# Kernel optimization log

Measured on AMD Instinct MI355X. Metric: run time of the kernel, lower is better.

Reference implementation:

```python
import jax, jax.numpy as jnp
import numpy as np


def setup_inputs() -> dict:
    key = jax.random.key(0)
    k1, k2, k3, k4 = jax.random.split(key, 4)
    B, D, C, N = 8192, 2048, 2048, 8
    x = jax.random.normal(k1, (B, D), dtype=jnp.float32)
    W = jax.random.normal(k2, (N, C, D), dtype=jnp.float32) * (1.0 / np.sqrt(D))
    b = jax.random.normal(k3, (N, C), dtype=jnp.float32) * 0.02
    factor = jnp.full((N,), 1.0 / N, dtype=jnp.float32)
    return {"x": x, "W": W, "b": b, "factor": factor}


def reference(x, W, b, factor):
    # Per-head linear: heads[b, n, c] = x @ W[n].T + b[n]
    heads = jnp.einsum("bd,ncd->bnc", x, W) + b[None, :, :]
    # Weighted sum over heads with canonical_factor (torch: cat(...,-1) @ factor)
    out = jnp.einsum("bnc,n->bc", heads, factor)
    return out
```

## Files before the change

### kernel.cpp

```cpp
#include <hip/hip_runtime.h>


#define MDIM 8192
#define KDIM 2048
#define NDIM 2048
#define NHEADS 8

#define BM 128
#define BN 128
#define BK 64

#define WBLKS 1024
#define XBLKS 1024
#define BBLKS 8

using bf16x8 = __attribute__((ext_vector_type(8))) short;
using f32x4  = __attribute__((ext_vector_type(4))) float;
using f4v    = __attribute__((ext_vector_type(4))) float;

__device__ __forceinline__ unsigned short f2bf(float x) {
    unsigned int u = __float_as_uint(x);
    u += 0x7FFFu + ((u >> 16) & 1u);
    return (unsigned short)(u >> 16);
}

__device__ __forceinline__ void async_load16(const void* g, void* l) {
    __builtin_amdgcn_global_load_lds(
        (const __attribute__((address_space(1))) unsigned int*)g,
        (__attribute__((address_space(3))) unsigned int*)l,
        16, 0, 0);
}

__global__ __launch_bounds__(256) void prep_kernel(
        const float* __restrict__ x,
        const float* __restrict__ W,
        const float* __restrict__ b,
        const float* __restrict__ factor,
        unsigned short* __restrict__ xbf,
        unsigned short* __restrict__ Wbf,
        float* __restrict__ beff) {
    const int blk = blockIdx.x;
    const int tid = threadIdx.x;
    if (blk < WBLKS) {
        const size_t CD   = (size_t)NDIM * KDIM;
        const int    nthr = WBLKS * 256;
        const int    c0   = blk * 256 + tid;
        float f[NHEADS];
#pragma unroll
        for (int n = 0; n < NHEADS; ++n) f[n] = factor[n];
        f4v v[4][NHEADS];
#pragma unroll
        for (int it = 0; it < 4; ++it) {
            size_t idx = ((size_t)(c0 + it * nthr)) * 4;
#pragma unroll
            for (int n = 0; n < NHEADS; ++n)
                v[it][n] = __builtin_nontemporal_load(
                    reinterpret_cast<const f4v*>(W + (size_t)n * CD + idx));
        }
#pragma unroll
        for (int it = 0; it < 4; ++it) {
            size_t idx = ((size_t)(c0 + it * nthr)) * 4;
            float ax = 0.f, ay = 0.f, az = 0.f, aw = 0.f;
#pragma unroll
            for (int n = 0; n < NHEADS; ++n) {
                ax += f[n] * v[it][n].x; ay += f[n] * v[it][n].y;
                az += f[n] * v[it][n].z; aw += f[n] * v[it][n].w;
            }
            ushort4 o;
            o.x = f2bf(ax); o.y = f2bf(ay); o.z = f2bf(az); o.w = f2bf(aw);
            *reinterpret_cast<ushort4*>(Wbf + idx) = o;
        }
    } else if (blk < WBLKS + XBLKS) {
        const int nthr = XBLKS * 256;
        const int c0   = (blk - WBLKS) * 256 + tid;
#pragma unroll
        for (int it = 0; it < 16; it += 4) {
            f4v v[4];
#pragma unroll
            for (int j = 0; j < 4; ++j)
                v[j] = *reinterpret_cast<const f4v*>(
                    x + ((size_t)(c0 + (it + j) * nthr)) * 4);
#pragma unroll
            for (int j = 0; j < 4; ++j) {
                size_t idx = ((size_t)(c0 + (it + j) * nthr)) * 4;
                ushort4 o;
                o.x = f2bf(v[j].x); o.y = f2bf(v[j].y);
                o.z = f2bf(v[j].z); o.w = f2bf(v[j].w);
                *reinterpret_cast<ushort4*>(xbf + idx) = o;
            }
        }
    } else {
        int c = (blk - WBLKS - XBLKS) * 256 + tid;
        float s = 0.f;
#pragma unroll
        for (int n = 0; n < NHEADS; ++n) s += factor[n] * b[(size_t)n * NDIM + c];
        beff[c] = s;
    }
}

__global__ __launch_bounds__(256) void gemm_bt_kernel(
    const unsigned short* __restrict__ A,
    const unsigned short* __restrict__ B,
    const float* __restrict__ bias,
    float* __restrict__ C)
{
    __shared__ unsigned short As[BM * BK];
    __shared__ unsigned short Bs[BN * BK];

    const int tid  = threadIdx.x;
    const int lane = tid & 63;
    const int w    = tid >> 6;
    const int m16  = lane & 15;
    const int quad = lane >> 4;

    const int bid = blockIdx.x;
    const int g   = bid >> 3;
    const int nt  = (bid & 7) * 2 + (g & 1);
    const int mt  = g >> 1;
    const int blockN0 = nt * BN;
    const int blockM0 = mt * BM;

    const int wr = (w >> 1) * 64;
    const int wc = (w & 1) * 64;

    const int srow = lane >> 3;
    const int scol = ((lane & 7) ^ srow) * 8;
    const unsigned short* aP[4];
    const unsigned short* bP[4];
    unsigned short* aL[4];
    unsigned short* bL[4];
#pragma unroll
    for (int i = 0; i < 4; ++i) {
        int r = i * 32 + w * 8;
        aP[i] = A + (size_t)(blockM0 + r + srow) * KDIM + scol;
        bP[i] = B + (size_t)(blockN0 + r + srow) * KDIM + scol;
        aL[i] = As + (size_t)r * BK;
        bL[i] = Bs + (size_t)r * BK;
    }

    f32x4 acc[4][4] = {};

    for (int k0 = 0; k0 < KDIM; k0 += BK) {
#pragma unroll
        for (int i = 0; i < 4; ++i) {
            async_load16(aP[i], aL[i]);
            async_load16(bP[i], bL[i]);
            aP[i] += BK; bP[i] += BK;
        }
        __syncthreads();

#pragma unroll
        for (int kk = 0; kk < BK; kk += 32) {
            bf16x8 af[4], bfr[4];
#pragma unroll
            for (int rt = 0; rt < 4; ++rt) {
                int row = wr + rt * 16 + m16;
                int gA = ((kk >> 3) + quad) ^ (row & 7);
                af[rt] = *reinterpret_cast<const bf16x8*>(&As[(size_t)row * BK + gA * 8]);
            }
#pragma unroll
            for (int ct = 0; ct < 4; ++ct) {
                int row = wc + ct * 16 + m16;
                int gB = ((kk >> 3) + quad) ^ (row & 7);
                bfr[ct] = *reinterpret_cast<const bf16x8*>(&Bs[(size_t)row * BK + gB * 8]);
            }
#pragma unroll
            for (int rt = 0; rt < 4; ++rt)
#pragma unroll
                for (int ct = 0; ct < 4; ++ct)
                    acc[rt][ct] = __builtin_amdgcn_mfma_f32_16x16x32_bf16(
                        af[rt], bfr[ct], acc[rt][ct], 0, 0, 0);
        }
        __syncthreads();
    }

    float bv[4];
#pragma unroll
    for (int ct = 0; ct < 4; ++ct) bv[ct] = bias[blockN0 + wc + ct * 16 + m16];
#pragma unroll
    for (int rt = 0; rt < 4; ++rt) {
        int row0 = blockM0 + wr + rt * 16 + quad * 4;
#pragma unroll
        for (int ct = 0; ct < 4; ++ct) {
            int col = blockN0 + wc + ct * 16 + m16;
#pragma unroll
            for (int r = 0; r < 4; ++r)
                C[(size_t)(row0 + r) * NDIM + col] = acc[rt][ct][r] + bv[ct];
        }
    }
}

extern "C" void kernel_launch(void* const* d_in, const int* in_sizes, int n_in,
                              void* d_out, int out_size, void* d_ws, size_t ws_size,
                              hipStream_t stream) {
    const float* x      = (const float*)d_in[0];
    const float* W      = (const float*)d_in[1];
    const float* b      = (const float*)d_in[2];
    const float* factor = (const float*)d_in[3];
    float* out = (float*)d_out;

    unsigned short* xbf  = (unsigned short*)d_ws;
    unsigned short* Wbf  = (unsigned short*)((char*)d_ws + 33554432);
    float*          beff = (float*)((char*)d_ws + 33554432 + 8388608);

    prep_kernel<<<dim3(WBLKS + XBLKS + BBLKS), dim3(256), 0, stream>>>(
        x, W, b, factor, xbf, Wbf, beff);
    gemm_bt_kernel<<<dim3(1024), dim3(256), 0, stream>>>(xbf, Wbf, beff, out);
}
```

Baseline: 325.9 us.

## Triple-buffer GEMM LDS tiles with 256x128 blocks and 512 threads

Rewrites the bf16 GEMM around a 3-stage LDS ring that prefetches two K-tiles ahead using async global-to-LDS loads. It replaces the two __syncthreads per iteration with one vmcnt wait plus a barrier, so memory latency overlaps the MFMA work. The block tile grows to 256x128 with 8 waves of 8x2 MFMA tiles each, giving more reuse per loaded tile. The nontemporal hint is also dropped from the W loads in the prep kernel. The ring uses about 147KB of LDS, which limits each CU to one block and leaves only 512 blocks in the grid.

```diff
diff --git a/kernel.cpp b/kernel.cpp
--- a/kernel.cpp
+++ b/kernel.cpp
@@ -6,9 +6,12 @@
 #define NDIM 2048
 #define NHEADS 8
 
-#define BM 128
+#define BM 256
 #define BN 128
 #define BK 64
+#define NT (KDIM / BK)
+#define ABUF_ELEMS (BM * BK)
+#define BBUF_ELEMS (BN * BK)
 
 #define WBLKS 1024
 #define XBLKS 1024
@@ -54,8 +57,7 @@
             size_t idx = ((size_t)(c0 + it * nthr)) * 4;
 #pragma unroll
             for (int n = 0; n < NHEADS; ++n)
-                v[it][n] = __builtin_nontemporal_load(
-                    reinterpret_cast<const f4v*>(W + (size_t)n * CD + idx));
+                v[it][n] = *reinterpret_cast<const f4v*>(W + (size_t)n * CD + idx);
         }
 #pragma unroll
         for (int it = 0; it < 4; ++it) {
@@ -98,20 +100,21 @@
     }
 }
 
-__global__ __launch_bounds__(256) void gemm_bt_kernel(
+__global__ __launch_bounds__(512) void gemm_bt_kernel(
     const unsigned short* __restrict__ A,
     const unsigned short* __restrict__ B,
     const float* __restrict__ bias,
     float* __restrict__ C)
 {
-    __shared__ unsigned short As[BM * BK];
-    __shared__ unsigned short Bs[BN * BK];
+    __shared__ unsigned short ring[3][ABUF_ELEMS + BBUF_ELEMS];
 
     const int tid  = threadIdx.x;
     const int lane = tid & 63;
     const int w    = tid >> 6;
     const int m16  = lane & 15;
     const int quad = lane >> 4;
+    const int wm   = w >> 2;
+    const int wn   = w & 3;
 
     const int bid = blockIdx.x;
     const int g   = bid >> 3;
@@ -120,69 +123,89 @@
     const int blockN0 = nt * BN;
     const int blockM0 = mt * BM;
 
-    const int wr = (w >> 1) * 64;
-    const int wc = (w & 1) * 64;
-
     const int srow = lane >> 3;
     const int scol = ((lane & 7) ^ srow) * 8;
     const unsigned short* aP[4];
-    const unsigned short* bP[4];
-    unsigned short* aL[4];
-    unsigned short* bL[4];
-#pragma unroll
-    for (int i = 0; i < 4; ++i) {
-        int r = i * 32 + w * 8;
-        aP[i] = A + (size_t)(blockM0 + r + srow) * KDIM + scol;
-        bP[i] = B + (size_t)(blockN0 + r + srow) * KDIM + scol;
-        aL[i] = As + (size_t)r * BK;
-        bL[i] = Bs + (size_t)r * BK;
-    }
-
-    f32x4 acc[4][4] = {};
-
-    for (int k0 = 0; k0 < KDIM; k0 += BK) {
-#pragma unroll
-        for (int i = 0; i < 4; ++i) {
-            async_load16(aP[i], aL[i]);
-            async_load16(bP[i], bL[i]);
-            aP[i] += BK; bP[i] += BK;
-        }
-        __syncthreads();
-
-#pragma unroll
-        for (int kk = 0; kk < BK; kk += 32) {
-            bf16x8 af[4], bfr[4];
-#pragma unroll
-            for (int rt = 0; rt < 4; ++rt) {
-                int row = wr + rt * 16 + m16;
-                int gA = ((kk >> 3) + quad) ^ (row & 7);
-                af[rt] = *reinterpret_cast<const bf16x8*>(&As[(size_t)row * BK + gA * 8]);
-            }
-#pragma unroll
-            for (int ct = 0; ct < 4; ++ct) {
-                int row = wc + ct * 16 + m16;
-                int gB = ((kk >> 3) + quad) ^ (row & 7);
-                bfr[ct] = *reinterpret_cast<const bf16x8*>(&Bs[(size_t)row * BK + gB * 8]);
-            }
-#pragma unroll
-            for (int rt = 0; rt < 4; ++rt)
-#pragma unroll
-                for (int ct = 0; ct < 4; ++ct)
+    const unsigned short* bP[2];
+#pragma unroll
+    for (int i = 0; i < 4; ++i)
+        aP[i] = A + (size_t)(blockM0 + (i * 8 + w) * 8 + srow) * KDIM + scol;
+#pragma unroll
+    for (int j = 0; j < 2; ++j)
+        bP[j] = B + (size_t)(blockN0 + (j * 8 + w) * 8 + srow) * KDIM + scol;
+
+#pragma unroll
+    for (int tt = 0; tt < 2; ++tt) {
+        unsigned short* As_r = &ring[tt][0];
+        unsigned short* Bs_r = &ring[tt][ABUF_ELEMS];
+        const size_t kofs = (size_t)tt * BK;
+#pragma unroll
+        for (int i = 0; i < 4; ++i)
+            async_load16(aP[i] + kofs, As_r + (i * 8 + w) * 512);
+#pragma unroll
+        for (int j = 0; j < 2; ++j)
+            async_load16(bP[j] + kofs, Bs_r + (j * 8 + w) * 512);
+    }
+
+    f32x4 acc[8][2] = {};
+
+    for (int t = 0; t < NT; ++t) {
+        if (t == NT - 1) asm volatile("s_waitcnt vmcnt(0)" ::: "memory");
+        else             asm volatile("s_waitcnt vmcnt(6)" ::: "memory");
+        __builtin_amdgcn_s_barrier();
+        __builtin_amdgcn_sched_barrier(0);
+
+        if (t + 2 < NT) {
+            const int s2 = (t + 2) % 3;
+            unsigned short* As_r = &ring[s2][0];
+            unsigned short* Bs_r = &ring[s2][ABUF_ELEMS];
+            const size_t kofs = (size_t)(t + 2) * BK;
+#pragma unroll
+            for (int i = 0; i < 4; ++i)
+                async_load16(aP[i] + kofs, As_r + (i * 8 + w) * 512);
+#pragma unroll
+            for (int j = 0; j < 2; ++j)
+                async_load16(bP[j] + kofs, Bs_r + (j * 8 + w) * 512);
+        }
+        __builtin_amdgcn_sched_barrier(0);
+
+        const int s = t % 3;
+        const unsigned short* As_r = &ring[s][0];
+        const unsigned short* Bs_r = &ring[s][ABUF_ELEMS];
+#pragma unroll
+        for (int ks = 0; ks < 2; ++ks) {
+            const int G = ks * 4 + quad;
+            bf16x8 af[8], bfr[2];
+#pragma unroll
+            for (int rt = 0; rt < 8; ++rt) {
+                int row = wm * 128 + rt * 16 + m16;
+                int gA = G ^ (row & 7);
+                af[rt] = *reinterpret_cast<const bf16x8*>(&As_r[(size_t)row * BK + gA * 8]);
+            }
+#pragma unroll
+            for (int ct = 0; ct < 2; ++ct) {
+                int row = wn * 32 + ct * 16 + m16;
+                int gB = G ^ (row & 7);
+                bfr[ct] = *reinterpret_cast<const bf16x8*>(&Bs_r[(size_t)row * BK + gB * 8]);
+            }
+#pragma unroll
+            for (int rt = 0; rt < 8; ++rt)
+#pragma unroll
+                for (int ct = 0; ct < 2; ++ct)
                     acc[rt][ct] = __builtin_amdgcn_mfma_f32_16x16x32_bf16(
                         af[rt], bfr[ct], acc[rt][ct], 0, 0, 0);
         }
-        __syncthreads();
-    }
-
-    float bv[4];
-#pragma unroll
-    for (int ct = 0; ct < 4; ++ct) bv[ct] = bias[blockN0 + wc + ct * 16 + m16];
-#pragma unroll
-    for (int rt = 0; rt < 4; ++rt) {
-        int row0 = blockM0 + wr + rt * 16 + quad * 4;
-#pragma unroll
-        for (int ct = 0; ct < 4; ++ct) {
-            int col = blockN0 + wc + ct * 16 + m16;
+    }
+
+    float bv[2];
+#pragma unroll
+    for (int ct = 0; ct < 2; ++ct) bv[ct] = bias[blockN0 + wn * 32 + ct * 16 + m16];
+#pragma unroll
+    for (int rt = 0; rt < 8; ++rt) {
+        int row0 = blockM0 + wm * 128 + rt * 16 + quad * 4;
+#pragma unroll
+        for (int ct = 0; ct < 2; ++ct) {
+            int col = blockN0 + wn * 32 + ct * 16 + m16;
 #pragma unroll
             for (int r = 0; r < 4; ++r)
                 C[(size_t)(row0 + r) * NDIM + col] = acc[rt][ct][r] + bv[ct];
@@ -205,5 +228,5 @@
 
     prep_kernel<<<dim3(WBLKS + XBLKS + BBLKS), dim3(256), 0, stream>>>(
         x, W, b, factor, xbf, Wbf, beff);
-    gemm_bt_kernel<<<dim3(1024), dim3(256), 0, stream>>>(xbf, Wbf, beff, out);
-}
+    gemm_bt_kernel<<<dim3(512), dim3(512), 0, stream>>>(xbf, Wbf, beff, out);
+}
```

New measurement: 340.7 us. 4.6% more time.
